# Performance work log

Hardware: AMD Instinct MI355X
Metric: run time of the kernel (lower is better)

The kernel has to match this reference:

```python
import jax, jax.numpy as jnp
import numpy as np

SIGMA = 0.248
PRNUM = 6
P = 7.5
K = 3.0
ALPHA = 2.5


def _gauss_kernel():
    # 5x5 normalized Gaussian, replicated per channel for depthwise conv [O=3,I=1,5,5]
    x = jnp.arange(-2, 3, dtype=jnp.float32)
    x2, y2 = jnp.meshgrid(x, x, indexing='xy')
    k = jnp.exp(-(x2 ** 2 + y2 ** 2) / (2.0 * SIGMA ** 2))
    k = k / jnp.sum(k)
    return jnp.broadcast_to(k[None, None], (3, 1, 5, 5))


def _dwconv(x, k):
    # x: [3,H,W]; depthwise 5x5 conv, padding=2 (matches F.conv2d(..., padding=2, groups=3))
    return jax.lax.conv_general_dilated(
        x[None], k, window_strides=(1, 1), padding=[(2, 2), (2, 2)],
        feature_group_count=3, dimension_numbers=('NCHW', 'OIHW', 'NCHW'))[0]


def _down2(x):
    # torch bilinear align_corners=False at exact scale 0.5 == 2x2 average pooling
    c, h, w = x.shape
    return x.reshape(c, h // 2, 2, w // 2, 2).mean(axis=(2, 4))


def _up(x, hw):
    # torch bilinear align_corners=False upsample (half-pixel centers) == jax linear resize
    return jax.image.resize(x, (x.shape[0], hw[0], hw[1]), method='linear')


def _foveate(img, fixs):
    C, H, W = img.shape
    k = _gauss_kernel()
    # build Gaussian pyramid
    G = img
    pyr = [G]
    for _ in range(1, PRNUM):
        G = _down2(_dwconv(G, k))
        pyr.append(G)
    # re-expand each level back to full res (interpolate then blur at each step)
    As = [pyr[0]]
    for i in range(1, PRNUM):
        cur = pyr[i]
        for j in range(i):
            hw = (cur.shape[1] * 2, cur.shape[2] * 2) if j < i - 1 else (H, W)
            cur = _dwconv(_up(cur, hw), k)
        As.append(cur)
    As = jnp.stack(As)  # [prNum, 3, H, W]

    # radial eccentricity map (min distance over fixations)
    x = jnp.arange(W, dtype=jnp.float32)
    y = jnp.arange(H, dtype=jnp.float32)
    x2d, y2d = jnp.meshgrid(x, y, indexing='xy')  # each [H, W]
    d = jnp.sqrt((x2d[None] - fixs[:, 0, None, None]) ** 2 +
                 (y2d[None] - fixs[:, 1, None, None]) ** 2) / P
    theta = jnp.min(d, axis=0)
    R = ALPHA / (theta + ALPHA)

    Ts = [jnp.exp(-((2.0 ** (i - 3)) * R / SIGMA) ** 2 * K) for i in range(1, PRNUM)]
    Ts.append(jnp.zeros_like(R))

    om = np.minimum(np.sqrt(np.log(2.0) / K) / (2.0 ** np.arange(-2, 3)) * SIGMA, 1.0)
    omega = np.concatenate([om, [0.0]]).astype(np.float32)  # [prNum]

    layer_ind = jnp.zeros_like(R)
    for i in range(1, PRNUM):
        ind = (R >= omega[i]) & (R <= omega[i - 1])
        layer_ind = jnp.where(ind, jnp.float32(i), layer_ind)

    Bs = [(0.5 - Ts[i]) / (Ts[i - 1] - Ts[i] + 1e-5) for i in range(1, PRNUM)]

    Ms = []
    for i in range(PRNUM):
        base = jnp.ones_like(R) if i == 0 else 1.0 - Bs[i - 1]
        M = jnp.where(layer_ind == i, base, jnp.float32(0.0))
        if i < PRNUM - 1:
            M = jnp.where(layer_ind == i + 1, Bs[i], M)
        Ms.append(M)
    Ms = jnp.stack(Ms)  # [prNum, H, W]

    # blend: sum_p Ms[p] * As[p, c]
    im_fov = jnp.einsum('phw,pchw->chw', Ms, As)
    return im_fov


def setup_inputs() -> dict:
    key = jax.random.key(0)
    k1, k2 = jax.random.split(key)
    img = jax.random.uniform(k1, (3, 2048, 2048), dtype=jnp.float32) * 255.0
    fixs = jax.random.uniform(k2, (4, 2), dtype=jnp.float32) * 2048.0
    return {'img': img, 'fixs': fixs}


def reference(img, fixs):
    return _foveate(img, fixs)
```

## Files before the change

### kernel.cpp

```cpp
#include <hip/hip_runtime.h>
#include <math.h>

#define HW2048 (2048ull*2048ull)
typedef float f4 __attribute__((ext_vector_type(4)));
typedef float f2 __attribute__((ext_vector_type(2)));

struct BP {
  float P[4][3];
  float D2[5];
  float cc[5];
};

__device__ __forceinline__ int ladder5(float dd, const BP& bp) {
  return (dd >= bp.D2[0]) + (dd >= bp.D2[1]) + (dd >= bp.D2[2]) +
         (dd >= bp.D2[3]) + (dd >= bp.D2[4]);
}

__global__ __launch_bounds__(256) void downAll_k(const float* __restrict__ img,
                                                 float* __restrict__ C1,
                                                 float* __restrict__ p2,
                                                 float* __restrict__ p3,
                                                 float* __restrict__ p4,
                                                 float* __restrict__ p5) {
  __shared__ float t2[16][17];
  __shared__ float t3[8][9];
  __shared__ float t4a[4][5];
  int tx = threadIdx.x, ty = threadIdx.y;
  int X = blockIdx.x * 16 + tx;
  int Y = blockIdx.y * 16 + ty;
  int c = blockIdx.z;
  const float* ip = img + (size_t)c * HW2048 + (size_t)(4 * Y) * 2048 + 4 * X;
  f4 r0 = __builtin_nontemporal_load((const f4*)(ip));
  f4 r1 = __builtin_nontemporal_load((const f4*)(ip + 2048));
  f4 r2 = __builtin_nontemporal_load((const f4*)(ip + 4096));
  f4 r3 = __builtin_nontemporal_load((const f4*)(ip + 6144));
  float a00 = 0.25f * (r0.x + r0.y + r1.x + r1.y);
  float a01 = 0.25f * (r0.z + r0.w + r1.z + r1.w);
  float a10 = 0.25f * (r2.x + r2.y + r3.x + r3.y);
  float a11 = 0.25f * (r2.z + r2.w + r3.z + r3.w);
  float* cp = C1 + (size_t)c * 1048576 + (size_t)(2 * Y) * 1024 + 2 * X;
  f2 u; u.x = a00; u.y = a01; *(f2*)cp = u;
  f2 v; v.x = a10; v.y = a11; *(f2*)(cp + 1024) = v;
  float m = 0.25f * (a00 + a01 + a10 + a11);
  p2[((size_t)c * 512 + Y) * 512 + X] = m;
  t2[ty][tx] = m;
  __syncthreads();
  int tid = ty * 16 + tx;
  if (tid < 64) {
    int y = tid >> 3, x = tid & 7;
    float w = 0.25f * (t2[2*y][2*x] + t2[2*y][2*x+1] + t2[2*y+1][2*x] + t2[2*y+1][2*x+1]);
    p3[((size_t)c * 256 + blockIdx.y * 8 + y) * 256 + blockIdx.x * 8 + x] = w;
    t3[y][x] = w;
  }
  __syncthreads();
  if (tid < 16) {
    int y = tid >> 2, x = tid & 3;
    float w = 0.25f * (t3[2*y][2*x] + t3[2*y][2*x+1] + t3[2*y+1][2*x] + t3[2*y+1][2*x+1]);
    p4[((size_t)c * 128 + blockIdx.y * 4 + y) * 128 + blockIdx.x * 4 + x] = w;
    t4a[y][x] = w;
  }
  __syncthreads();
  if (tid < 4) {
    int y = tid >> 1, x = tid & 1;
    float w = 0.25f * (t4a[2*y][2*x] + t4a[2*y][2*x+1] + t4a[2*y+1][2*x] + t4a[2*y+1][2*x+1]);
    p5[((size_t)c * 64 + blockIdx.y * 2 + y) * 64 + blockIdx.x * 2 + x] = w;
  }
}

__device__ __forceinline__ void up_coords(int o, int n, int& i0, int& i1, float& w0) {
  int m = o >> 1;
  if (o & 1) { i0 = m; i1 = min(m + 1, n - 1); w0 = 0.75f; }
  else       { i0 = max(m - 1, 0); i1 = m;     w0 = 0.25f; }
}

__device__ __forceinline__ void s2c(const float* __restrict__ b, int x0, int y0,
                                    const BP& bp, float o[2][4]) {
  int t = x0 >> 2, ky = y0 >> 2, yph = y0 & 3;
  int c[3], r[3];
#pragma unroll
  for (int j = 0; j < 3; ++j) {
    c[j] = min(max(t - 1 + j, 0), 511);
    r[j] = min(max(ky - 1 + j, 0), 511);
  }
  float v[3][3];
#pragma unroll
  for (int j = 0; j < 3; ++j) {
    const float* row = b + r[j] * 512;
    v[j][0] = row[c[0]]; v[j][1] = row[c[1]]; v[j][2] = row[c[2]];
  }
  const float* wr0 = bp.P[yph];
  const float* wr1 = bp.P[yph + 1];
  float rv0[3], rv1[3];
#pragma unroll
  for (int i = 0; i < 3; ++i) {
    rv0[i] = wr0[0] * v[0][i] + wr0[1] * v[1][i] + wr0[2] * v[2][i];
    rv1[i] = wr1[0] * v[0][i] + wr1[1] * v[1][i] + wr1[2] * v[2][i];
  }
#pragma unroll
  for (int p = 0; p < 4; ++p) {
    o[0][p] = bp.P[p][0] * rv0[0] + bp.P[p][1] * rv0[1] + bp.P[p][2] * rv0[2];
    o[1][p] = bp.P[p][0] * rv1[0] + bp.P[p][1] * rv1[1] + bp.P[p][2] * rv1[2];
  }
}

__device__ __forceinline__ void s2c_lds(const float (*t)[68], int tx, int kyr, int yph,
                                        const BP& bp, float o[2][4]) {
  float v[3][3];
#pragma unroll
  for (int j = 0; j < 3; ++j) {
    const float* row = t[kyr + j];
    v[j][0] = row[tx]; v[j][1] = row[tx + 1]; v[j][2] = row[tx + 2];
  }
  const float* wr0 = bp.P[yph];
  const float* wr1 = bp.P[yph + 1];
  float rv0[3], rv1[3];
#pragma unroll
  for (int i = 0; i < 3; ++i) {
    rv0[i] = wr0[0] * v[0][i] + wr0[1] * v[1][i] + wr0[2] * v[2][i];
    rv1[i] = wr1[0] * v[0][i] + wr1[1] * v[1][i] + wr1[2] * v[2][i];
  }
#pragma unroll
  for (int p = 0; p < 4; ++p) {
    o[0][p] = bp.P[p][0] * rv0[0] + bp.P[p][1] * rv0[1] + bp.P[p][2] * rv0[2];
    o[1][p] = bp.P[p][0] * rv1[0] + bp.P[p][1] * rv1[1] + bp.P[p][2] * rv1[2];
  }
}

__device__ __forceinline__ void s1c(const float* __restrict__ b, int x0, int y0,
                                    float o[2][4]) {
  int q0 = x0 >> 1, qy = y0 >> 1;
  int c[4], r[3];
#pragma unroll
  for (int i = 0; i < 4; ++i) c[i] = min(max(q0 - 1 + i, 0), 1023);
#pragma unroll
  for (int j = 0; j < 3; ++j) r[j] = min(max(qy - 1 + j, 0), 1023);
  float v[3][4];
#pragma unroll
  for (int j = 0; j < 3; ++j) {
    const float* row = b + r[j] * 1024;
    v[j][0] = row[c[0]]; v[j][1] = row[c[1]]; v[j][2] = row[c[2]]; v[j][3] = row[c[3]];
  }
  float rv0[4], rv1[4];
#pragma unroll
  for (int i = 0; i < 4; ++i) {
    rv0[i] = 0.25f * v[0][i] + 0.75f * v[1][i];
    rv1[i] = 0.75f * v[1][i] + 0.25f * v[2][i];
  }
  o[0][0] = 0.25f * rv0[0] + 0.75f * rv0[1];
  o[0][1] = 0.75f * rv0[1] + 0.25f * rv0[2];
  o[0][2] = 0.25f * rv0[1] + 0.75f * rv0[2];
  o[0][3] = 0.75f * rv0[2] + 0.25f * rv0[3];
  o[1][0] = 0.25f * rv1[0] + 0.75f * rv1[1];
  o[1][1] = 0.75f * rv1[1] + 0.25f * rv1[2];
  o[1][2] = 0.25f * rv1[1] + 0.75f * rv1[2];
  o[1][3] = 0.75f * rv1[2] + 0.25f * rv1[3];
}

__device__ __forceinline__ void sampleL(
    int l, int ch, int x0, int y0, int tx, int kyr,
    const float* __restrict__ img, const float* __restrict__ C1,
    const float* __restrict__ p2,
    const float (*tU)[3][4][68], const BP& bp, float o[2][4]) {
  if (l == 0) {
    const float* imgc = img + (size_t)ch * HW2048;
    f4 v0 = *(const f4*)(imgc + (size_t)y0 * 2048 + x0);
    f4 v1 = *(const f4*)(imgc + (size_t)(y0 + 1) * 2048 + x0);
    o[0][0] = v0.x; o[0][1] = v0.y; o[0][2] = v0.z; o[0][3] = v0.w;
    o[1][0] = v1.x; o[1][1] = v1.y; o[1][2] = v1.z; o[1][3] = v1.w;
  } else if (l == 1) {
    s1c(C1 + (size_t)ch * 1048576, x0, y0, o);
  } else if (l == 2) {
    s2c(p2 + (size_t)ch * 262144, x0, y0, bp, o);
  } else {
    s2c_lds(tU[ch][l - 3], tx, kyr, y0 & 3, bp, o);
  }
}

__global__ __launch_bounds__(256) void fblend_k(
    const float* __restrict__ img, const float* __restrict__ C1,
    const float* __restrict__ p2, const float* __restrict__ p3,
    const float* __restrict__ p4, const float* __restrict__ p5,
    const float* __restrict__ fixs, int nf,
    float* __restrict__ out, BP bp) {
  __shared__ float tU[3][3][4][68];
  __shared__ float tM[3][2][5][38];
  __shared__ float tA[3][5][22];

  int tx = threadIdx.x, ty = threadIdx.y;
  int bx = blockIdx.x, by = blockIdx.y;
  int xs = bx * 64 + tx;
  int yp = by * 4 + ty;
  int x0 = xs * 4, y0 = yp * 2;
  size_t ob0 = (size_t)y0 * 2048 + x0;

  int X0 = bx * 256, Y0 = by * 8;
  float bDmin = 3.4e38f, bDmax = 3.4e38f;
  for (int f = 0; f < nf; ++f) {
    float fx = fixs[2 * f], fy = fixs[2 * f + 1];
    float dxm = fmaxf(fmaxf((float)X0 - fx, fx - (float)(X0 + 255)), 0.f);
    float dym = fmaxf(fmaxf((float)Y0 - fy, fy - (float)(Y0 + 7)), 0.f);
    bDmin = fminf(bDmin, dxm * dxm + dym * dym);
    float dxM = fmaxf(fx - (float)X0, (float)(X0 + 255) - fx);
    float dyM = fmaxf(fy - (float)Y0, (float)(Y0 + 7) - fy);
    bDmax = fminf(bDmax, dxM * dxM + dyM * dyM);
  }
  int bLmax = ladder5(bDmax + 2.0f, bp);
  int bLmin = ladder5(fmaxf(bDmin - 2.0f, 0.f), bp);

  if (bLmax == 0) {
#pragma unroll
    for (int ch = 0; ch < 3; ++ch) {
      const float* imgc = img + (size_t)ch * HW2048;
      f4 v0 = *(const f4*)(imgc + ob0);
      f4 v1 = *(const f4*)(imgc + ob0 + 2048);
      __builtin_nontemporal_store(v0, (f4*)(out + (size_t)ch * HW2048 + ob0));
      __builtin_nontemporal_store(v1, (f4*)(out + (size_t)ch * HW2048 + ob0 + 2048));
    }
    return;
  }

  int sLo = max(bLmin - 1, 3), sHi = min(bLmax, 5);
  int g0 = 2 * by - 1, c0 = 64 * bx - 1;
  if (sLo <= sHi) {
    int m0 = (g0 >> 1) - 1, n0 = (c0 >> 1) - 1;
    int q0 = (m0 >> 1) - 1, s0 = (n0 >> 1) - 1;
    bool lv5 = (sHi == 5), lv4 = (sLo <= 4 && sHi >= 4), lv3 = (sLo == 3);

    if (lv5) {
      if (tx < 20) {
#pragma unroll
        for (int rr = 0; rr < 2; ++rr) {
          int r = (rr == 0) ? ty : 4;
          if (rr == 0 || ty == 0) {
            int gy = min(max(q0 + r, 0), 127);
            int gx = min(max(s0 + tx, 0), 127);
            int r0, r1, e0, e1; float wy0, wx0;
            up_coords(gy, 64, r0, r1, wy0);
            up_coords(gx, 64, e0, e1, wx0);
            float wy1 = 1.f - wy0, wx1 = 1.f - wx0;
            int i00 = r0*64+e0, i01 = r0*64+e1, i10 = r1*64+e0, i11 = r1*64+e1;
#pragma unroll
            for (int ch = 0; ch < 3; ++ch) {
              const float* s = p5 + ch * 4096;
              tA[ch][r][tx] = wy0 * (wx0 * s[i00] + wx1 * s[i01])
                            + wy1 * (wx0 * s[i10] + wx1 * s[i11]);
            }
          }
        }
      }
      __syncthreads();
    }

    if (lv4 || lv5) {
      if (tx < 36) {
#pragma unroll
        for (int rr = 0; rr < 2; ++rr) {
          int r = (rr == 0) ? ty : 4;
          if (rr == 0 || ty == 0) {
            int gy = min(max(m0 + r, 0), 255);
            int gx = min(max(n0 + tx, 0), 255);
            int r0, r1, e0, e1; float wy0, wx0;
            up_coords(gy, 128, r0, r1, wy0);
            up_coords(gx, 128, e0, e1, wx0);
            float wy1 = 1.f - wy0, wx1 = 1.f - wx0;
            if (lv4) {
              int i00 = r0*128+e0, i01 = r0*128+e1, i10 = r1*128+e0, i11 = r1*128+e1;
#pragma unroll
              for (int ch = 0; ch < 3; ++ch) {
                const float* s = p4 + ch * 16384;
                tM[ch][0][r][tx] = wy0 * (wx0 * s[i00] + wx1 * s[i01])
                                 + wy1 * (wx0 * s[i10] + wx1 * s[i11]);
              }
            }
            if (lv5) {
              int a0 = r0 - q0, a1 = r1 - q0, b0 = e0 - s0, b1 = e1 - s0;
#pragma unroll
              for (int ch = 0; ch < 3; ++ch)
                tM[ch][1][r][tx] = wy0 * (wx0 * tA[ch][a0][b0] + wx1 * tA[ch][a0][b1])
                                 + wy1 * (wx0 * tA[ch][a1][b0] + wx1 * tA[ch][a1][b1]);
            }
          }
        }
      }
      __syncthreads();
    }

    {
#pragma unroll
      for (int cc2 = 0; cc2 < 2; ++cc2) {
        int cI = (cc2 == 0) ? tx : 64 + tx;
        if (cc2 == 0 || tx < 2) {
          int gy = min(max(g0 + ty, 0), 511);
          int gx = min(max(c0 + cI, 0), 511);
          int r0, r1, e0, e1; float wy0, wx0;
          up_coords(gy, 256, r0, r1, wy0);
          up_coords(gx, 256, e0, e1, wx0);
          float wy1 = 1.f - wy0, wx1 = 1.f - wx0;
          if (lv3) {
            int i00 = r0*256+e0, i01 = r0*256+e1, i10 = r1*256+e0, i11 = r1*256+e1;
#pragma unroll
            for (int ch = 0; ch < 3; ++ch) {
              const float* s = p3 + ch * 65536;
              tU[ch][0][ty][cI] = wy0 * (wx0 * s[i00] + wx1 * s[i01])
                                + wy1 * (wx0 * s[i10] + wx1 * s[i11]);
            }
          }
          int a0 = r0 - m0, a1 = r1 - m0, b0 = e0 - n0, b1 = e1 - n0;
          if (lv4) {
#pragma unroll
            for (int ch = 0; ch < 3; ++ch)
              tU[ch][1][ty][cI] = wy0 * (wx0 * tM[ch][0][a0][b0] + wx1 * tM[ch][0][a0][b1])
                                + wy1 * (wx0 * tM[ch][0][a1][b0] + wx1 * tM[ch][0][a1][b1]);
          }
          if (lv5) {
#pragma unroll
            for (int ch = 0; ch < 3; ++ch)
              tU[ch][2][ty][cI] = wy0 * (wx0 * tM[ch][1][a0][b0] + wx1 * tM[ch][1][a0][b1])
                                + wy1 * (wx0 * tM[ch][1][a1][b0] + wx1 * tM[ch][1][a1][b1]);
          }
        }
      }
      __syncthreads();
    }
  }

  float d2[2][4];
#pragma unroll
  for (int j = 0; j < 2; ++j)
#pragma unroll
    for (int i = 0; i < 4; ++i) d2[j][i] = 3.4e38f;
  for (int f = 0; f < nf; ++f) {
    float dx0 = (float)x0 - fixs[2 * f], dy0 = (float)y0 - fixs[2 * f + 1];
#pragma unroll
    for (int j = 0; j < 2; ++j) {
      float dy = dy0 + (float)j, dy2 = dy * dy;
#pragma unroll
      for (int i = 0; i < 4; ++i) {
        float dx = dx0 + (float)i;
        d2[j][i] = fminf(d2[j][i], dx * dx + dy2);
      }
    }
  }

  bool uniformB = (bLmin == bLmax);
  int lmax;
  bool mixed;
  if (uniformB) {
    lmax = bLmax; mixed = false;
  } else {
    float dmn = d2[0][0], dmx = d2[0][0];
#pragma unroll
    for (int j = 0; j < 2; ++j)
#pragma unroll
      for (int i = 0; i < 4; ++i) {
        dmn = fminf(dmn, d2[j][i]);
        dmx = fmaxf(dmx, d2[j][i]);
      }
    lmax = ladder5(dmx, bp);
    int lmin = ladder5(dmn, bp);
    mixed = (lmin != lmax);
  }

  if (lmax == 0) {
#pragma unroll
    for (int ch = 0; ch < 3; ++ch) {
      const float* imgc = img + (size_t)ch * HW2048;
      f4 v0 = *(const f4*)(imgc + ob0);
      f4 v1 = *(const f4*)(imgc + ob0 + 2048);
      __builtin_nontemporal_store(v0, (f4*)(out + (size_t)ch * HW2048 + ob0));
      __builtin_nontemporal_store(v1, (f4*)(out + (size_t)ch * HW2048 + ob0 + 2048));
    }
    return;
  }

  float thr  = (lmax == 1) ? bp.D2[0] : (lmax == 2) ? bp.D2[1] :
               (lmax == 3) ? bp.D2[2] : (lmax == 4) ? bp.D2[3] : bp.D2[4];
  float cm_A = (lmax == 1) ? bp.cc[0] : (lmax == 2) ? bp.cc[1] :
               (lmax == 3) ? bp.cc[2] : (lmax == 4) ? bp.cc[3] : bp.cc[4];
  float cm_B = (lmax <= 2) ? bp.cc[0] : (lmax == 3) ? bp.cc[1] :
               (lmax == 4) ? bp.cc[2] : bp.cc[3];
  bool top5 = (lmax >= 5);

  float Bv[2][4];
  bool  tp[2][4];
#pragma unroll
  for (int j = 0; j < 2; ++j)
#pragma unroll
    for (int i = 0; i < 4; ++i) {
      float dd = d2[j][i];
      bool top = uniformB ? true : (dd >= thr);
      tp[j][i] = top;
      float d = dd * __frsqrt_rn(dd);
      float R = 18.75f * __frcp_rn(d + 18.75f);
      float R2 = R * R;
      float cm = top ? cm_A : cm_B;
      float tsm = __expf(-cm * R2);
      float t2 = tsm * tsm;
      float tsL = (top && top5) ? 0.f : t2 * t2;
      float B = (0.5f - tsL) * __frcp_rn(tsm - tsL + 1e-5f);
      if (!top && lmax == 1) B = 0.f;
      Bv[j][i] = B;
    }

  int kyr = ty >> 1;
#pragma unroll
  for (int ch = 0; ch < 3; ++ch) {
    float sA[2][4], sB[2][4], sC[2][4];
    sampleL(lmax,     ch, x0, y0, tx, kyr, img, C1, p2, tU, bp, sA);
    sampleL(lmax - 1, ch, x0, y0, tx, kyr, img, C1, p2, tU, bp, sB);
#pragma unroll
    for (int j = 0; j < 2; ++j)
#pragma unroll
      for (int i = 0; i < 4; ++i) sC[j][i] = sB[j][i];
    if (mixed && lmax >= 2)
      sampleL(lmax - 2, ch, x0, y0, tx, kyr, img, C1, p2, tU, bp, sC);

    float res[2][4];
#pragma unroll
    for (int j = 0; j < 2; ++j)
#pragma unroll
      for (int i = 0; i < 4; ++i) {
        float B = Bv[j][i];
        bool top = tp[j][i];
        float hi = top ? sA[j][i] : sB[j][i];
        float lo = top ? sB[j][i] : sC[j][i];
        res[j][i] = B * lo + (1.f - B) * hi;
      }

    f4 v0, v1;
    v0.x = res[0][0]; v0.y = res[0][1]; v0.z = res[0][2]; v0.w = res[0][3];
    v1.x = res[1][0]; v1.y = res[1][1]; v1.z = res[1][2]; v1.w = res[1][3];
    __builtin_nontemporal_store(v0, (f4*)(out + (size_t)ch * HW2048 + ob0));
    __builtin_nontemporal_store(v1, (f4*)(out + (size_t)ch * HW2048 + ob0 + 2048));
  }
}

extern "C" void kernel_launch(void* const* d_in, const int* in_sizes, int n_in,
                              void* d_out, int out_size, void* d_ws, size_t ws_size,
                              hipStream_t stream) {
  const float* img  = (const float*)d_in[0];
  const float* fixs = (const float*)d_in[1];
  int nf = in_sizes[1] / 2;
  float* out = (float*)d_out;
  float* ws  = (float*)d_ws;

  BP bp;
  const double sig = 0.248, Kd = 3.0, Pd = 7.5, Ad = 2.5;
  double obv = sqrt(log(2.0) / Kd) * sig;
  for (int j = 0; j < 5; ++j) {
    double om = obv * pow(2.0, 2 - j);
    double Dj = Pd * Ad * (1.0 / om - 1.0);
    bp.D2[j] = (float)(Dj * Dj);
  }
  for (int X = 0; X < 5; ++X)
    bp.cc[X] = (float)(Kd * pow(2.0, 2.0 * (X - 2)) / (sig * sig));
  const float Pt[4][3] = {{0.375f, 0.625f, 0.f},
                          {0.1875f, 0.75f, 0.0625f},
                          {0.0625f, 0.75f, 0.1875f},
                          {0.f, 0.625f, 0.375f}};
  for (int a = 0; a < 4; ++a) for (int t = 0; t < 3; ++t) bp.P[a][t] = Pt[a][t];

  size_t o = 0;
  float* C1 = ws + o; o += 3ull * 1024 * 1024;
  float* p2 = ws + o; o += 3ull * 512 * 512;
  float* p3 = ws + o; o += 3ull * 256 * 256;
  float* p4 = ws + o; o += 3ull * 128 * 128;
  float* p5 = ws + o; o += 3ull * 64 * 64;

  downAll_k <<<dim3(32, 32, 3), dim3(16, 16), 0, stream>>>(img, C1, p2, p3, p4, p5);
  fblend_k  <<<dim3(8, 256),    dim3(64, 4),  0, stream>>>(img, C1, p2, p3, p4, p5,
                                                           fixs, nf, out, bp);
}
```

Baseline: 131.1 us.

## Skip level-1 writes far from fixations and restage upsample chain with fewer barriers

The downsample kernel now computes, per 64x64 block, the minimum squared distance to any fixation. It writes the level-1 pyramid (C1) only when that distance is within a radius (the level-3 threshold plus a margin), since blocks farther away never read that level. The blend kernel's shared-memory upsampling stages are regrouped by dependency depth, so independent levels fill in the same phase. The number of barriers stays at three, but they are now unconditional. The skip relies on the margin correctly covering the blend kernel's read footprint.

Result: faster. 128.5 us (-2.0%).

```diff
diff --git a/kernel.cpp b/kernel.cpp
--- a/kernel.cpp
+++ b/kernel.cpp
@@ -21,7 +21,9 @@
                                                  float* __restrict__ p2,
                                                  float* __restrict__ p3,
                                                  float* __restrict__ p4,
-                                                 float* __restrict__ p5) {
+                                                 float* __restrict__ p5,
+                                                 const float* __restrict__ fixs,
+                                                 int nf, float c1thr) {
   __shared__ float t2[16][17];
   __shared__ float t3[8][9];
   __shared__ float t4a[4][5];
@@ -29,6 +31,17 @@
   int X = blockIdx.x * 16 + tx;
   int Y = blockIdx.y * 16 + ty;
   int c = blockIdx.z;
+
+  int XB = blockIdx.x * 64, YB = blockIdx.y * 64;
+  float bD = 3.4e38f;
+  for (int f = 0; f < nf; ++f) {
+    float fx = fixs[2 * f], fy = fixs[2 * f + 1];
+    float dx = fmaxf(fmaxf((float)XB - fx, fx - (float)(XB + 63)), 0.f);
+    float dy = fmaxf(fmaxf((float)YB - fy, fy - (float)(YB + 63)), 0.f);
+    bD = fminf(bD, dx * dx + dy * dy);
+  }
+  bool wC1 = (bD <= c1thr);
+
   const float* ip = img + (size_t)c * HW2048 + (size_t)(4 * Y) * 2048 + 4 * X;
   f4 r0 = __builtin_nontemporal_load((const f4*)(ip));
   f4 r1 = __builtin_nontemporal_load((const f4*)(ip + 2048));
@@ -38,9 +51,11 @@
   float a01 = 0.25f * (r0.z + r0.w + r1.z + r1.w);
   float a10 = 0.25f * (r2.x + r2.y + r3.x + r3.y);
   float a11 = 0.25f * (r2.z + r2.w + r3.z + r3.w);
-  float* cp = C1 + (size_t)c * 1048576 + (size_t)(2 * Y) * 1024 + 2 * X;
-  f2 u; u.x = a00; u.y = a01; *(f2*)cp = u;
-  f2 v; v.x = a10; v.y = a11; *(f2*)(cp + 1024) = v;
+  if (wC1) {
+    float* cp = C1 + (size_t)c * 1048576 + (size_t)(2 * Y) * 1024 + 2 * X;
+    f2 u; u.x = a00; u.y = a01; *(f2*)cp = u;
+    f2 v; v.x = a10; v.y = a11; *(f2*)(cp + 1024) = v;
+  }
   float m = 0.25f * (a00 + a01 + a10 + a11);
   p2[((size_t)c * 512 + Y) * 512 + X] = m;
   t2[ty][tx] = m;
@@ -226,66 +241,49 @@
     int q0 = (m0 >> 1) - 1, s0 = (n0 >> 1) - 1;
     bool lv5 = (sHi == 5), lv4 = (sLo <= 4 && sHi >= 4), lv3 = (sLo == 3);
 
-    if (lv5) {
-      if (tx < 20) {
-#pragma unroll
-        for (int rr = 0; rr < 2; ++rr) {
-          int r = (rr == 0) ? ty : 4;
-          if (rr == 0 || ty == 0) {
-            int gy = min(max(q0 + r, 0), 127);
-            int gx = min(max(s0 + tx, 0), 127);
-            int r0, r1, e0, e1; float wy0, wx0;
-            up_coords(gy, 64, r0, r1, wy0);
-            up_coords(gx, 64, e0, e1, wx0);
-            float wy1 = 1.f - wy0, wx1 = 1.f - wx0;
-            int i00 = r0*64+e0, i01 = r0*64+e1, i10 = r1*64+e0, i11 = r1*64+e1;
-#pragma unroll
-            for (int ch = 0; ch < 3; ++ch) {
-              const float* s = p5 + ch * 4096;
-              tA[ch][r][tx] = wy0 * (wx0 * s[i00] + wx1 * s[i01])
-                            + wy1 * (wx0 * s[i10] + wx1 * s[i11]);
-            }
+    if (lv5 && tx < 20) {
+#pragma unroll
+      for (int rr = 0; rr < 2; ++rr) {
+        int r = (rr == 0) ? ty : 4;
+        if (rr == 0 || ty == 0) {
+          int gy = min(max(q0 + r, 0), 127);
+          int gx = min(max(s0 + tx, 0), 127);
+          int r0, r1, e0, e1; float wy0, wx0;
+          up_coords(gy, 64, r0, r1, wy0);
+          up_coords(gx, 64, e0, e1, wx0);
+          float wy1 = 1.f - wy0, wx1 = 1.f - wx0;
+          int i00 = r0*64+e0, i01 = r0*64+e1, i10 = r1*64+e0, i11 = r1*64+e1;
+#pragma unroll
+          for (int ch = 0; ch < 3; ++ch) {
+            const float* s = p5 + ch * 4096;
+            tA[ch][r][tx] = wy0 * (wx0 * s[i00] + wx1 * s[i01])
+                          + wy1 * (wx0 * s[i10] + wx1 * s[i11]);
           }
         }
       }
-      __syncthreads();
-    }
-
-    if (lv4 || lv5) {
-      if (tx < 36) {
-#pragma unroll
-        for (int rr = 0; rr < 2; ++rr) {
-          int r = (rr == 0) ? ty : 4;
-          if (rr == 0 || ty == 0) {
-            int gy = min(max(m0 + r, 0), 255);
-            int gx = min(max(n0 + tx, 0), 255);
-            int r0, r1, e0, e1; float wy0, wx0;
-            up_coords(gy, 128, r0, r1, wy0);
-            up_coords(gx, 128, e0, e1, wx0);
-            float wy1 = 1.f - wy0, wx1 = 1.f - wx0;
-            if (lv4) {
-              int i00 = r0*128+e0, i01 = r0*128+e1, i10 = r1*128+e0, i11 = r1*128+e1;
-#pragma unroll
-              for (int ch = 0; ch < 3; ++ch) {
-                const float* s = p4 + ch * 16384;
-                tM[ch][0][r][tx] = wy0 * (wx0 * s[i00] + wx1 * s[i01])
-                                 + wy1 * (wx0 * s[i10] + wx1 * s[i11]);
-              }
-            }
-            if (lv5) {
-              int a0 = r0 - q0, a1 = r1 - q0, b0 = e0 - s0, b1 = e1 - s0;
-#pragma unroll
-              for (int ch = 0; ch < 3; ++ch)
-                tM[ch][1][r][tx] = wy0 * (wx0 * tA[ch][a0][b0] + wx1 * tA[ch][a0][b1])
-                                 + wy1 * (wx0 * tA[ch][a1][b0] + wx1 * tA[ch][a1][b1]);
-            }
+    }
+    if (lv4 && tx < 36) {
+#pragma unroll
+      for (int rr = 0; rr < 2; ++rr) {
+        int r = (rr == 0) ? ty : 4;
+        if (rr == 0 || ty == 0) {
+          int gy = min(max(m0 + r, 0), 255);
+          int gx = min(max(n0 + tx, 0), 255);
+          int r0, r1, e0, e1; float wy0, wx0;
+          up_coords(gy, 128, r0, r1, wy0);
+          up_coords(gx, 128, e0, e1, wx0);
+          float wy1 = 1.f - wy0, wx1 = 1.f - wx0;
+          int i00 = r0*128+e0, i01 = r0*128+e1, i10 = r1*128+e0, i11 = r1*128+e1;
+#pragma unroll
+          for (int ch = 0; ch < 3; ++ch) {
+            const float* s = p4 + ch * 16384;
+            tM[ch][0][r][tx] = wy0 * (wx0 * s[i00] + wx1 * s[i01])
+                             + wy1 * (wx0 * s[i10] + wx1 * s[i11]);
           }
         }
       }
-      __syncthreads();
-    }
-
-    {
+    }
+    if (lv3) {
 #pragma unroll
       for (int cc2 = 0; cc2 < 2; ++cc2) {
         int cI = (cc2 == 0) ? tx : 64 + tx;
@@ -296,32 +294,78 @@
           up_coords(gy, 256, r0, r1, wy0);
           up_coords(gx, 256, e0, e1, wx0);
           float wy1 = 1.f - wy0, wx1 = 1.f - wx0;
-          if (lv3) {
-            int i00 = r0*256+e0, i01 = r0*256+e1, i10 = r1*256+e0, i11 = r1*256+e1;
-#pragma unroll
-            for (int ch = 0; ch < 3; ++ch) {
-              const float* s = p3 + ch * 65536;
-              tU[ch][0][ty][cI] = wy0 * (wx0 * s[i00] + wx1 * s[i01])
-                                + wy1 * (wx0 * s[i10] + wx1 * s[i11]);
-            }
-          }
-          int a0 = r0 - m0, a1 = r1 - m0, b0 = e0 - n0, b1 = e1 - n0;
-          if (lv4) {
-#pragma unroll
-            for (int ch = 0; ch < 3; ++ch)
-              tU[ch][1][ty][cI] = wy0 * (wx0 * tM[ch][0][a0][b0] + wx1 * tM[ch][0][a0][b1])
-                                + wy1 * (wx0 * tM[ch][0][a1][b0] + wx1 * tM[ch][0][a1][b1]);
-          }
-          if (lv5) {
-#pragma unroll
-            for (int ch = 0; ch < 3; ++ch)
-              tU[ch][2][ty][cI] = wy0 * (wx0 * tM[ch][1][a0][b0] + wx1 * tM[ch][1][a0][b1])
-                                + wy1 * (wx0 * tM[ch][1][a1][b0] + wx1 * tM[ch][1][a1][b1]);
+          int i00 = r0*256+e0, i01 = r0*256+e1, i10 = r1*256+e0, i11 = r1*256+e1;
+#pragma unroll
+          for (int ch = 0; ch < 3; ++ch) {
+            const float* s = p3 + ch * 65536;
+            tU[ch][0][ty][cI] = wy0 * (wx0 * s[i00] + wx1 * s[i01])
+                              + wy1 * (wx0 * s[i10] + wx1 * s[i11]);
           }
         }
       }
-      __syncthreads();
-    }
+    }
+    __syncthreads();
+
+    if (lv5 && tx < 36) {
+#pragma unroll
+      for (int rr = 0; rr < 2; ++rr) {
+        int r = (rr == 0) ? ty : 4;
+        if (rr == 0 || ty == 0) {
+          int gy = min(max(m0 + r, 0), 255);
+          int gx = min(max(n0 + tx, 0), 255);
+          int r0, r1, e0, e1; float wy0, wx0;
+          up_coords(gy, 128, r0, r1, wy0);
+          up_coords(gx, 128, e0, e1, wx0);
+          float wy1 = 1.f - wy0, wx1 = 1.f - wx0;
+          int a0 = r0 - q0, a1 = r1 - q0, b0 = e0 - s0, b1 = e1 - s0;
+#pragma unroll
+          for (int ch = 0; ch < 3; ++ch)
+            tM[ch][1][r][tx] = wy0 * (wx0 * tA[ch][a0][b0] + wx1 * tA[ch][a0][b1])
+                             + wy1 * (wx0 * tA[ch][a1][b0] + wx1 * tA[ch][a1][b1]);
+        }
+      }
+    }
+    if (lv4) {
+#pragma unroll
+      for (int cc2 = 0; cc2 < 2; ++cc2) {
+        int cI = (cc2 == 0) ? tx : 64 + tx;
+        if (cc2 == 0 || tx < 2) {
+          int gy = min(max(g0 + ty, 0), 511);
+          int gx = min(max(c0 + cI, 0), 511);
+          int r0, r1, e0, e1; float wy0, wx0;
+          up_coords(gy, 256, r0, r1, wy0);
+          up_coords(gx, 256, e0, e1, wx0);
+          float wy1 = 1.f - wy0, wx1 = 1.f - wx0;
+          int a0 = r0 - m0, a1 = r1 - m0, b0 = e0 - n0, b1 = e1 - n0;
+#pragma unroll
+          for (int ch = 0; ch < 3; ++ch)
+            tU[ch][1][ty][cI] = wy0 * (wx0 * tM[ch][0][a0][b0] + wx1 * tM[ch][0][a0][b1])
+                              + wy1 * (wx0 * tM[ch][0][a1][b0] + wx1 * tM[ch][0][a1][b1]);
+        }
+      }
+    }
+    __syncthreads();
+
+    if (lv5) {
+#pragma unroll
+      for (int cc2 = 0; cc2 < 2; ++cc2) {
+        int cI = (cc2 == 0) ? tx : 64 + tx;
+        if (cc2 == 0 || tx < 2) {
+          int gy = min(max(g0 + ty, 0), 511);
+          int gx = min(max(c0 + cI, 0), 511);
+          int r0, r1, e0, e1; float wy0, wx0;
+          up_coords(gy, 256, r0, r1, wy0);
+          up_coords(gx, 256, e0, e1, wx0);
+          float wy1 = 1.f - wy0, wx1 = 1.f - wx0;
+          int a0 = r0 - m0, a1 = r1 - m0, b0 = e0 - n0, b1 = e1 - n0;
+#pragma unroll
+          for (int ch = 0; ch < 3; ++ch)
+            tU[ch][2][ty][cI] = wy0 * (wx0 * tM[ch][1][a0][b0] + wx1 * tM[ch][1][a0][b1])
+                              + wy1 * (wx0 * tM[ch][1][a1][b0] + wx1 * tM[ch][1][a1][b1]);
+        }
+      }
+    }
+    __syncthreads();
   }
 
   float d2[2][4];
@@ -460,6 +504,9 @@
                           {0.f, 0.625f, 0.375f}};
   for (int a = 0; a < 4; ++a) for (int t = 0; t < 3; ++t) bp.P[a][t] = Pt[a][t];
 
+  double rC1 = sqrt((double)bp.D2[3]) + 16.0;
+  float c1thr = (float)(rC1 * rC1);
+
   size_t o = 0;
   float* C1 = ws + o; o += 3ull * 1024 * 1024;
   float* p2 = ws + o; o += 3ull * 512 * 512;
@@ -467,7 +514,8 @@
   float* p4 = ws + o; o += 3ull * 128 * 128;
   float* p5 = ws + o; o += 3ull * 64 * 64;
 
-  downAll_k <<<dim3(32, 32, 3), dim3(16, 16), 0, stream>>>(img, C1, p2, p3, p4, p5);
+  downAll_k <<<dim3(32, 32, 3), dim3(16, 16), 0, stream>>>(img, C1, p2, p3, p4, p5,
+                                                           fixs, nf, c1thr);
   fblend_k  <<<dim3(8, 256),    dim3(64, 4),  0, stream>>>(img, C1, p2, p3, p4, p5,
                                                            fixs, nf, out, bp);
 }
```
